# Optimization experiments

Hardware: AMD Instinct MI355X
Metric: run time of the kernel (lower is better)

Reference implementation:

```python
import jax, jax.numpy as jnp
import numpy as np

TAU = 2.0  # self.temperature
EPS = 1e-7

def setup_inputs() -> dict:
    key = jax.random.key(0)
    k1, k2, k3, k4, k5, k6 = jax.random.split(key, 6)
    B, S, H = 8, 4096, 512
    G, V, Dg = 2, 320, 128  # groups, codevectors per group, codevector_dim // G
    hidden_states = jax.random.normal(k1, (B, S, H), dtype=jnp.float32)
    mask_time_indices = jax.random.randint(k2, (B, S), 0, 2) > 0
    u = jax.random.uniform(k3, (B * S, G, V), dtype=jnp.float32, minval=1e-6, maxval=1.0 - 1e-6)
    gumbel_noise = -jnp.log(-jnp.log(u))  # standard Gumbel samples, as in F.gumbel_softmax
    W_proj = jax.random.normal(k4, (H, G * V), dtype=jnp.float32) * 0.02
    b_proj = jax.random.normal(k5, (G * V,), dtype=jnp.float32) * 0.02
    codevectors = jax.random.normal(k6, (G, V, Dg), dtype=jnp.float32)
    return {"hidden_states": hidden_states, "mask_time_indices": mask_time_indices,
            "gumbel_noise": gumbel_noise, "W_proj": W_proj, "b_proj": b_proj,
            "codevectors": codevectors}

def reference(hidden_states, mask_time_indices, gumbel_noise, W_proj, b_proj, codevectors):
    B, S, H = hidden_states.shape
    G, V, Dg = codevectors.shape
    N = B * S
    # weight projection: [B,S,H] -> [B,S,G*V] -> [N, G, V]
    logits = (jnp.einsum('bsh,hk->bsk', hidden_states, W_proj) + b_proj)
    logits = logits.reshape(N, G, V).astype(jnp.float32)
    # gumbel-softmax with hard=True (straight-through)
    y_soft = jax.nn.softmax((logits + gumbel_noise) / TAU, axis=-1)  # [N,G,V]
    idx = jnp.argmax(y_soft, axis=-1)                                 # [N,G]
    y_hard = jax.nn.one_hot(idx, V, dtype=y_soft.dtype)
    codevector_probs = y_hard + y_soft - jax.lax.stop_gradient(y_soft)
    # perplexity on the (noise-free) soft distribution, masked marginal
    soft_dist = jax.nn.softmax(logits, axis=-1)                       # [N,G,V]
    m = mask_time_indices.reshape(-1).astype(jnp.float32)             # [N]
    marginal = jnp.einsum('ngv,n->gv', soft_dist, m) / jnp.sum(m)
    perplexity = jnp.sum(jnp.exp(-jnp.sum(marginal * jnp.log(marginal + EPS), axis=-1)))
    # hard one-hot weighted sum over codebook == gather of selected codevector
    cv = jnp.einsum('ngv,gvd->ngd', codevector_probs, codevectors)    # [N,G,Dg]
    cv = cv.reshape(B, S, G * Dg)
    return cv, perplexity
```

## Files before the change

kernel.cpp:

```cpp
#include <hip/hip_runtime.h>
#include <hip/hip_bf16.h>
#include <math.h>

#define N_ROWS 32768
#define H      512
#define GV     640
#define V      320
#define DG     128
#define BM     32
#define NT     16

typedef __attribute__((ext_vector_type(4))) float f32x4;
typedef __attribute__((ext_vector_type(8))) short short8v;

static __device__ __forceinline__ short f2bf(float f) {
    unsigned int u = __float_as_uint(f);
    u += 0x7fffu + ((u >> 16) & 1u);
    return (short)(u >> 16);
}

__global__ __launch_bounds__(256)
void pack_w(const float* __restrict__ W, short* __restrict__ wp)
{
    int gid = blockIdx.x * 256 + threadIdx.x;
    int l   = gid & 63;
    int ct  = (gid >> 6) % 40;
    int t   = gid / (40 * 64);
    int row = t * 32 + 8 * (l >> 4);
    int col = ct * 16 + (l & 15);
    short8v pk;
    #pragma unroll
    for (int i = 0; i < 8; ++i)
        pk[i] = f2bf(W[(size_t)(row + i) * GV + col]);
    *(short8v*)(wp + (size_t)gid * 8) = pk;
}

__global__ __launch_bounds__(256)
void pack_a(const float* __restrict__ hidden, short* __restrict__ ap)
{
    int gid = blockIdx.x * 256 + threadIdx.x;
    int l   = gid & 63;
    int t   = (gid >> 6) & 15;
    int rt  = gid >> 10;
    const float* src = hidden + (size_t)(rt * 16 + (l & 15)) * H + t * 32 + 8 * (l >> 4);
    float4 x0 = *(const float4*)src;
    float4 x1 = *(const float4*)(src + 4);
    short8v pk;
    pk[0] = f2bf(x0.x); pk[1] = f2bf(x0.y); pk[2] = f2bf(x0.z); pk[3] = f2bf(x0.w);
    pk[4] = f2bf(x1.x); pk[5] = f2bf(x1.y); pk[6] = f2bf(x1.z); pk[7] = f2bf(x1.w);
    *(short8v*)(ap + (size_t)gid * 8) = pk;
}

__global__ __launch_bounds__(512, 4)
void gumbel_vq_main(const short* apack,
                    const int*   __restrict__ mask,
                    const float* __restrict__ gumbel,
                    const short* __restrict__ wpack,
                    const float* __restrict__ bias,
                    const float* __restrict__ codevec,
                    float* out,
                    float* __restrict__ ws)
{
    __shared__ __align__(16) short sbuf[2][20480];
    float4 (*ex)[16]  = (float4 (*)[16])(&sbuf[0][0]);
    float*  ex2       = (float*)((char*)sbuf + 2048);
    float*  mg        = (float*)((char*)sbuf + 2560);
    int   (*rowtab)[2] = (int (*)[2])((char*)sbuf + 7680);

    const int tid = threadIdx.x;
    const int tn  = tid & 63;
    const int wid = tid >> 6;
    const int wm  = wid >> 2;
    const int wn  = wid & 3;
    const int q   = tn >> 4;
    const int cn  = tn & 15;
    const int row0 = blockIdx.x * BM;
    const int cbase = wn * 160 + cn;

    f32x4 acc[10];
    #pragma unroll
    for (int j = 0; j < 10; ++j) {
        float b = bias[cbase + j * 16];
        f32x4 c; c[0] = b; c[1] = b; c[2] = b; c[3] = b;
        acc[j] = c;
    }

    const short* ab = apack + ((size_t)(blockIdx.x * 2 + wm) * NT * 64 + tn) * 8;

    {
        const short* wt = wpack;
        short8v s0 = *(const short8v*)(wt + (size_t)(tid +    0) * 8);
        short8v s1 = *(const short8v*)(wt + (size_t)(tid +  512) * 8);
        short8v s2 = *(const short8v*)(wt + (size_t)(tid + 1024) * 8);
        short8v s3 = *(const short8v*)(wt + (size_t)(tid + 1536) * 8);
        short8v s4 = *(const short8v*)(wt + (size_t)(tid + 2048) * 8);
        short* bd = &sbuf[0][(size_t)tid * 8];
        *(short8v*)(bd +     0) = s0;
        *(short8v*)(bd +  4096) = s1;
        *(short8v*)(bd +  8192) = s2;
        *(short8v*)(bd + 12288) = s3;
        *(short8v*)(bd + 16384) = s4;
    }
    short8v areg = *(const short8v*)ab;
    __syncthreads();

    #pragma unroll
    for (int t = 0; t < NT; ++t) {
        const int cur = t & 1;
        short8v s0, s1, s2, s3, s4, anx;
        if (t + 1 < NT) {
            const short* wt = wpack + (size_t)(t + 1) * 20480;
            s0 = *(const short8v*)(wt + (size_t)(tid +    0) * 8);
            s1 = *(const short8v*)(wt + (size_t)(tid +  512) * 8);
            s2 = *(const short8v*)(wt + (size_t)(tid + 1024) * 8);
            s3 = *(const short8v*)(wt + (size_t)(tid + 1536) * 8);
            s4 = *(const short8v*)(wt + (size_t)(tid + 2048) * 8);
            anx = *(const short8v*)(ab + (size_t)(t + 1) * 512);
        }
        const short* bufc = &sbuf[cur][(size_t)(wn * 640 + tn) * 8];
        #pragma unroll
        for (int j = 0; j < 10; ++j) {
            short8v bf = *(const short8v*)(bufc + j * 512);
            acc[j] = __builtin_amdgcn_mfma_f32_16x16x32_bf16(areg, bf, acc[j], 0, 0, 0);
        }
        if (t + 1 < NT) {
            short* bd = &sbuf[cur ^ 1][(size_t)tid * 8];
            *(short8v*)(bd +     0) = s0;
            *(short8v*)(bd +  4096) = s1;
            *(short8v*)(bd +  8192) = s2;
            *(short8v*)(bd + 12288) = s3;
            *(short8v*)(bd + 16384) = s4;
            areg = anx;
        }
        __syncthreads();
    }

    float g[4][10];
    #pragma unroll
    for (int r = 0; r < 4; ++r) {
        const float* gp = gumbel + (size_t)(row0 + wm * 16 + 4 * q + r) * GV + cbase;
        #pragma unroll
        for (int j = 0; j < 10; ++j) g[r][j] = gp[j * 16];
    }
    float mrow[4];
    #pragma unroll
    for (int r = 0; r < 4; ++r)
        mrow[r] = (mask[row0 + wm * 16 + 4 * q + r] != 0) ? 1.f : 0.f;

    float lm[4];
    #pragma unroll
    for (int r = 0; r < 4; ++r) {
        lm[r] = acc[0][r];
        #pragma unroll
        for (int j = 1; j < 10; ++j) lm[r] = fmaxf(lm[r], acc[j][r]);
    }
    #pragma unroll
    for (int d = 8; d >= 1; d >>= 1)
        #pragma unroll
        for (int r = 0; r < 4; ++r)
            lm[r] = fmaxf(lm[r], __shfl_xor(lm[r], d, 64));

    float zm[4]; int zi[4];
    #pragma unroll
    for (int r = 0; r < 4; ++r) {
        zm[r] = acc[0][r] + g[r][0]; zi[r] = cbase;
        #pragma unroll
        for (int j = 1; j < 10; ++j) {
            float zj = acc[j][r] + g[r][j];
            if (zj > zm[r]) { zm[r] = zj; zi[r] = cbase + 16 * j; }
        }
    }
    #pragma unroll
    for (int d = 8; d >= 1; d >>= 1) {
        #pragma unroll
        for (int r = 0; r < 4; ++r) {
            float oz = __shfl_xor(zm[r], d, 64); int oi = __shfl_xor(zi[r], d, 64);
            if (oz > zm[r] || (oz == zm[r] && oi < zi[r])) { zm[r] = oz; zi[r] = oi; }
        }
    }

    if (cn == 0) {
        #pragma unroll
        for (int r = 0; r < 4; ++r) {
            float4 e; e.x = zm[r]; e.y = __int_as_float(zi[r]); e.z = lm[r]; e.w = 0.f;
            ex[wid][4 * q + r] = e;
        }
    }
    __syncthreads();
    const int pw = wid ^ 1;
    #pragma unroll
    for (int r = 0; r < 4; ++r) {
        float4 e = ex[pw][4 * q + r];
        float pz = e.x; int pi = __float_as_int(e.y);
        if (pz > zm[r] || (pz == zm[r] && pi < zi[r])) { zm[r] = pz; zi[r] = pi; }
        lm[r] = fmaxf(lm[r], e.z);
    }

    float pm[4][10], ps[4];
    #pragma unroll
    for (int r = 0; r < 4; ++r) {
        ps[r] = 0.f;
        #pragma unroll
        for (int j = 0; j < 10; ++j) {
            float p = __expf(acc[j][r] - lm[r]);
            pm[r][j] = p; ps[r] += p;
        }
    }
    #pragma unroll
    for (int d = 8; d >= 1; d >>= 1)
        #pragma unroll
        for (int r = 0; r < 4; ++r)
            ps[r] += __shfl_xor(ps[r], d, 64);

    if (cn == 0) {
        #pragma unroll
        for (int r = 0; r < 4; ++r) ex2[wid * 16 + 4 * q + r] = ps[r];
    }
    __syncthreads();
    float inv[4];
    #pragma unroll
    for (int r = 0; r < 4; ++r)
        inv[r] = mrow[r] / (ps[r] + ex2[pw * 16 + 4 * q + r]);

    float part[10];
    #pragma unroll
    for (int j = 0; j < 10; ++j) {
        part[j] = pm[0][j] * inv[0] + pm[1][j] * inv[1] + pm[2][j] * inv[2] + pm[3][j] * inv[3];
        part[j] += __shfl_xor(part[j], 16, 64);
        part[j] += __shfl_xor(part[j], 32, 64);
    }
    if (q == 0) {
        #pragma unroll
        for (int j = 0; j < 10; ++j)
            mg[wm * GV + cbase + 16 * j] = part[j];
    }
    if ((wn == 0 || wn == 2) && cn == 0) {
        int grp = wn >> 1;
        #pragma unroll
        for (int r = 0; r < 4; ++r)
            rowtab[wm * 16 + 4 * q + r][grp] = zi[r] - grp * V;
    }
    __syncthreads();

    for (int c = tid; c < GV; c += 512)
        atomicAdd(&ws[c], mg[c] + mg[GV + c]);
    if (wid == 0) {
        int mr = (tn < BM) ? (mask[row0 + tn] != 0) : 0;
        unsigned long long b = __ballot(mr);
        if (tn == 0) atomicAdd(&ws[GV], (float)__popcll(b));
    }
    {
        const int row = tid >> 4;
        const int six = tid & 15;
        #pragma unroll
        for (int i = 0; i < 4; ++i) {
            int e4  = six + 16 * i;
            int grp = e4 >> 5;
            int off = e4 & 31;
            int idx = rowtab[row][grp];
            float4 vv = ((const float4*)(codevec + ((size_t)grp * V + idx) * DG))[off];
            ((float4*)(out + (size_t)(row0 + row) * (2 * DG)))[e4] = vv;
        }
    }
}

__global__ void gumbel_vq_finalize(const float* __restrict__ ws, float* __restrict__ out)
{
    __shared__ float red[GV];
    int t = threadIdx.x;
    float cnt = ws[GV];
    float p = ws[t] / cnt;
    red[t] = p * logf(p + 1e-7f);
    __syncthreads();
    if (t == 0) {
        float e0 = 0.f, e1 = 0.f;
        for (int i = 0; i < V; ++i)  e0 += red[i];
        for (int i = V; i < GV; ++i) e1 += red[i];
        out[(size_t)N_ROWS * 2 * DG] = expf(-e0) + expf(-e1);
    }
}

extern "C" void kernel_launch(void* const* d_in, const int* in_sizes, int n_in,
                              void* d_out, int out_size, void* d_ws, size_t ws_size,
                              hipStream_t stream)
{
    const float* hidden  = (const float*)d_in[0];
    const int*   mask    = (const int*)  d_in[1];
    const float* gumbel  = (const float*)d_in[2];
    const float* W       = (const float*)d_in[3];
    const float* bias    = (const float*)d_in[4];
    const float* codevec = (const float*)d_in[5];
    float* out = (float*)d_out;
    float* ws  = (float*)d_ws;
    short* wpack = (short*)((char*)d_ws + 4096);
    short* apack = (short*)d_out;

    hipMemsetAsync(d_ws, 0, (GV + 1) * sizeof(float), stream);
    pack_w<<<160, 256, 0, stream>>>(W, wpack);
    pack_a<<<8192, 256, 0, stream>>>(hidden, apack);
    gumbel_vq_main<<<N_ROWS / BM, 512, 0, stream>>>(apack, mask, gumbel, wpack, bias, codevec, out, ws);
    gumbel_vq_finalize<<<1, GV, 0, stream>>>(ws, out);
}
```

Baseline: 102.4 us.

## Process two 16-row tiles per wave to reuse LDS weight fragments

Doubles the rows per block from 32 to 64. Each wave now keeps two accumulator sets and runs two MFMAs on every weight fragment it reads from LDS, so the full packed weight matrix is streamed through LDS half as often per row. The softmax, argmax and marginal epilogue is looped over the two row tiles, and the codevector gather is remapped to cover 64 rows. The cost is more accumulator registers, which may lower occupancy, and half as many blocks to spread across CUs.

```diff
diff --git a/kernel.cpp b/kernel.cpp
--- a/kernel.cpp
+++ b/kernel.cpp
@@ -7,7 +7,7 @@
 #define GV     640
 #define V      320
 #define DG     128
-#define BM     32
+#define BM     64
 #define NT     16
 
 typedef __attribute__((ext_vector_type(4))) float f32x4;
@@ -62,9 +62,9 @@
                     float* __restrict__ ws)
 {
     __shared__ __align__(16) short sbuf[2][20480];
-    float4 (*ex)[16]  = (float4 (*)[16])(&sbuf[0][0]);
-    float*  ex2       = (float*)((char*)sbuf + 2048);
-    float*  mg        = (float*)((char*)sbuf + 2560);
+    float4 (*ex)[16]   = (float4 (*)[16])(&sbuf[0][0]);
+    float*  ex2        = (float*)((char*)sbuf + 2048);
+    float*  mg         = (float*)((char*)sbuf + 2560);
     int   (*rowtab)[2] = (int (*)[2])((char*)sbuf + 7680);
 
     const int tid = threadIdx.x;
@@ -77,15 +77,16 @@
     const int row0 = blockIdx.x * BM;
     const int cbase = wn * 160 + cn;
 
-    f32x4 acc[10];
+    f32x4 acc[2][10];
     #pragma unroll
     for (int j = 0; j < 10; ++j) {
         float b = bias[cbase + j * 16];
         f32x4 c; c[0] = b; c[1] = b; c[2] = b; c[3] = b;
-        acc[j] = c;
-    }
-
-    const short* ab = apack + ((size_t)(blockIdx.x * 2 + wm) * NT * 64 + tn) * 8;
+        acc[0][j] = c; acc[1][j] = c;
+    }
+
+    const short* ab0 = apack + ((size_t)(blockIdx.x * 4 + wm * 2) * 1024 + tn) * 8;
+    const short* ab1 = ab0 + (size_t)1024 * 8;
 
     {
         const short* wt = wpack;
@@ -101,13 +102,14 @@
         *(short8v*)(bd + 12288) = s3;
         *(short8v*)(bd + 16384) = s4;
     }
-    short8v areg = *(const short8v*)ab;
+    short8v areg0 = *(const short8v*)ab0;
+    short8v areg1 = *(const short8v*)ab1;
     __syncthreads();
 
     #pragma unroll
     for (int t = 0; t < NT; ++t) {
         const int cur = t & 1;
-        short8v s0, s1, s2, s3, s4, anx;
+        short8v s0, s1, s2, s3, s4, an0, an1;
         if (t + 1 < NT) {
             const short* wt = wpack + (size_t)(t + 1) * 20480;
             s0 = *(const short8v*)(wt + (size_t)(tid +    0) * 8);
@@ -115,13 +117,15 @@
             s2 = *(const short8v*)(wt + (size_t)(tid + 1024) * 8);
             s3 = *(const short8v*)(wt + (size_t)(tid + 1536) * 8);
             s4 = *(const short8v*)(wt + (size_t)(tid + 2048) * 8);
-            anx = *(const short8v*)(ab + (size_t)(t + 1) * 512);
+            an0 = *(const short8v*)(ab0 + (size_t)(t + 1) * 512);
+            an1 = *(const short8v*)(ab1 + (size_t)(t + 1) * 512);
         }
         const short* bufc = &sbuf[cur][(size_t)(wn * 640 + tn) * 8];
         #pragma unroll
         for (int j = 0; j < 10; ++j) {
             short8v bf = *(const short8v*)(bufc + j * 512);
-            acc[j] = __builtin_amdgcn_mfma_f32_16x16x32_bf16(areg, bf, acc[j], 0, 0, 0);
+            acc[0][j] = __builtin_amdgcn_mfma_f32_16x16x32_bf16(areg0, bf, acc[0][j], 0, 0, 0);
+            acc[1][j] = __builtin_amdgcn_mfma_f32_16x16x32_bf16(areg1, bf, acc[1][j], 0, 0, 0);
         }
         if (t + 1 < NT) {
             short* bd = &sbuf[cur ^ 1][(size_t)tid * 8];
@@ -130,102 +134,120 @@
             *(short8v*)(bd +  8192) = s2;
             *(short8v*)(bd + 12288) = s3;
             *(short8v*)(bd + 16384) = s4;
-            areg = anx;
+            areg0 = an0; areg1 = an1;
         }
         __syncthreads();
     }
 
-    float g[4][10];
-    #pragma unroll
-    for (int r = 0; r < 4; ++r) {
-        const float* gp = gumbel + (size_t)(row0 + wm * 16 + 4 * q + r) * GV + cbase;
-        #pragma unroll
-        for (int j = 0; j < 10; ++j) g[r][j] = gp[j * 16];
-    }
-    float mrow[4];
-    #pragma unroll
-    for (int r = 0; r < 4; ++r)
-        mrow[r] = (mask[row0 + wm * 16 + 4 * q + r] != 0) ? 1.f : 0.f;
-
-    float lm[4];
-    #pragma unroll
-    for (int r = 0; r < 4; ++r) {
-        lm[r] = acc[0][r];
-        #pragma unroll
-        for (int j = 1; j < 10; ++j) lm[r] = fmaxf(lm[r], acc[j][r]);
-    }
-    #pragma unroll
-    for (int d = 8; d >= 1; d >>= 1)
+    float part[10];
+    #pragma unroll
+    for (int j = 0; j < 10; ++j) part[j] = 0.f;
+    const int pw = wid ^ 1;
+
+    #pragma unroll
+    for (int rt = 0; rt < 2; ++rt) {
+        const int rowbase = row0 + wm * 32 + rt * 16;
+
+        float g[4][10];
+        #pragma unroll
+        for (int r = 0; r < 4; ++r) {
+            const float* gp = gumbel + (size_t)(rowbase + 4 * q + r) * GV + cbase;
+            #pragma unroll
+            for (int j = 0; j < 10; ++j) g[r][j] = gp[j * 16];
+        }
+        float mrow[4];
         #pragma unroll
         for (int r = 0; r < 4; ++r)
-            lm[r] = fmaxf(lm[r], __shfl_xor(lm[r], d, 64));
-
-    float zm[4]; int zi[4];
-    #pragma unroll
-    for (int r = 0; r < 4; ++r) {
-        zm[r] = acc[0][r] + g[r][0]; zi[r] = cbase;
-        #pragma unroll
-        for (int j = 1; j < 10; ++j) {
-            float zj = acc[j][r] + g[r][j];
-            if (zj > zm[r]) { zm[r] = zj; zi[r] = cbase + 16 * j; }
-        }
-    }
-    #pragma unroll
-    for (int d = 8; d >= 1; d >>= 1) {
-        #pragma unroll
-        for (int r = 0; r < 4; ++r) {
-            float oz = __shfl_xor(zm[r], d, 64); int oi = __shfl_xor(zi[r], d, 64);
-            if (oz > zm[r] || (oz == zm[r] && oi < zi[r])) { zm[r] = oz; zi[r] = oi; }
-        }
-    }
-
-    if (cn == 0) {
-        #pragma unroll
-        for (int r = 0; r < 4; ++r) {
-            float4 e; e.x = zm[r]; e.y = __int_as_float(zi[r]); e.z = lm[r]; e.w = 0.f;
-            ex[wid][4 * q + r] = e;
-        }
-    }
-    __syncthreads();
-    const int pw = wid ^ 1;
-    #pragma unroll
-    for (int r = 0; r < 4; ++r) {
-        float4 e = ex[pw][4 * q + r];
-        float pz = e.x; int pi = __float_as_int(e.y);
-        if (pz > zm[r] || (pz == zm[r] && pi < zi[r])) { zm[r] = pz; zi[r] = pi; }
-        lm[r] = fmaxf(lm[r], e.z);
-    }
-
-    float pm[4][10], ps[4];
-    #pragma unroll
-    for (int r = 0; r < 4; ++r) {
-        ps[r] = 0.f;
-        #pragma unroll
-        for (int j = 0; j < 10; ++j) {
-            float p = __expf(acc[j][r] - lm[r]);
-            pm[r][j] = p; ps[r] += p;
-        }
-    }
-    #pragma unroll
-    for (int d = 8; d >= 1; d >>= 1)
+            mrow[r] = (mask[rowbase + 4 * q + r] != 0) ? 1.f : 0.f;
+
+        float lm[4];
+        #pragma unroll
+        for (int r = 0; r < 4; ++r) {
+            lm[r] = acc[rt][0][r];
+            #pragma unroll
+            for (int j = 1; j < 10; ++j) lm[r] = fmaxf(lm[r], acc[rt][j][r]);
+        }
+        #pragma unroll
+        for (int d = 8; d >= 1; d >>= 1)
+            #pragma unroll
+            for (int r = 0; r < 4; ++r)
+                lm[r] = fmaxf(lm[r], __shfl_xor(lm[r], d, 64));
+
+        float zm[4]; int zi[4];
+        #pragma unroll
+        for (int r = 0; r < 4; ++r) {
+            zm[r] = acc[rt][0][r] + g[r][0]; zi[r] = cbase;
+            #pragma unroll
+            for (int j = 1; j < 10; ++j) {
+                float zj = acc[rt][j][r] + g[r][j];
+                if (zj > zm[r]) { zm[r] = zj; zi[r] = cbase + 16 * j; }
+            }
+        }
+        #pragma unroll
+        for (int d = 8; d >= 1; d >>= 1) {
+            #pragma unroll
+            for (int r = 0; r < 4; ++r) {
+                float oz = __shfl_xor(zm[r], d, 64); int oi = __shfl_xor(zi[r], d, 64);
+                if (oz > zm[r] || (oz == zm[r] && oi < zi[r])) { zm[r] = oz; zi[r] = oi; }
+            }
+        }
+
+        if (cn == 0) {
+            #pragma unroll
+            for (int r = 0; r < 4; ++r) {
+                float4 e; e.x = zm[r]; e.y = __int_as_float(zi[r]); e.z = lm[r]; e.w = 0.f;
+                ex[wid][4 * q + r] = e;
+            }
+        }
+        __syncthreads();
+        #pragma unroll
+        for (int r = 0; r < 4; ++r) {
+            float4 e = ex[pw][4 * q + r];
+            float pz = e.x; int pi = __float_as_int(e.y);
+            if (pz > zm[r] || (pz == zm[r] && pi < zi[r])) { zm[r] = pz; zi[r] = pi; }
+            lm[r] = fmaxf(lm[r], e.z);
+        }
+
+        float pm[4][10], ps[4];
+        #pragma unroll
+        for (int r = 0; r < 4; ++r) {
+            ps[r] = 0.f;
+            #pragma unroll
+            for (int j = 0; j < 10; ++j) {
+                float p = __expf(acc[rt][j][r] - lm[r]);
+                pm[r][j] = p; ps[r] += p;
+            }
+        }
+        #pragma unroll
+        for (int d = 8; d >= 1; d >>= 1)
+            #pragma unroll
+            for (int r = 0; r < 4; ++r)
+                ps[r] += __shfl_xor(ps[r], d, 64);
+
+        if (cn == 0) {
+            #pragma unroll
+            for (int r = 0; r < 4; ++r) ex2[wid * 16 + 4 * q + r] = ps[r];
+        }
+        __syncthreads();
+        float inv[4];
         #pragma unroll
         for (int r = 0; r < 4; ++r)
-            ps[r] += __shfl_xor(ps[r], d, 64);
-
-    if (cn == 0) {
-        #pragma unroll
-        for (int r = 0; r < 4; ++r) ex2[wid * 16 + 4 * q + r] = ps[r];
-    }
-    __syncthreads();
-    float inv[4];
-    #pragma unroll
-    for (int r = 0; r < 4; ++r)
-        inv[r] = mrow[r] / (ps[r] + ex2[pw * 16 + 4 * q + r]);
-
-    float part[10];
+            inv[r] = mrow[r] / (ps[r] + ex2[pw * 16 + 4 * q + r]);
+
+        #pragma unroll
+        for (int j = 0; j < 10; ++j)
+            part[j] += pm[0][j] * inv[0] + pm[1][j] * inv[1] + pm[2][j] * inv[2] + pm[3][j] * inv[3];
+
+        if ((wn == 0 || wn == 2) && cn == 0) {
+            int grp = wn >> 1;
+            #pragma unroll
+            for (int r = 0; r < 4; ++r)
+                rowtab[wm * 32 + rt * 16 + 4 * q + r][grp] = zi[r] - grp * V;
+        }
+    }
+
     #pragma unroll
     for (int j = 0; j < 10; ++j) {
-        part[j] = pm[0][j] * inv[0] + pm[1][j] * inv[1] + pm[2][j] * inv[2] + pm[3][j] * inv[3];
         part[j] += __shfl_xor(part[j], 16, 64);
         part[j] += __shfl_xor(part[j], 32, 64);
     }
@@ -233,28 +255,22 @@
         #pragma unroll
         for (int j = 0; j < 10; ++j)
             mg[wm * GV + cbase + 16 * j] = part[j];
-    }
-    if ((wn == 0 || wn == 2) && cn == 0) {
-        int grp = wn >> 1;
-        #pragma unroll
-        for (int r = 0; r < 4; ++r)
-            rowtab[wm * 16 + 4 * q + r][grp] = zi[r] - grp * V;
     }
     __syncthreads();
 
     for (int c = tid; c < GV; c += 512)
         atomicAdd(&ws[c], mg[c] + mg[GV + c]);
     if (wid == 0) {
-        int mr = (tn < BM) ? (mask[row0 + tn] != 0) : 0;
+        int mr = (mask[row0 + tn] != 0);
         unsigned long long b = __ballot(mr);
         if (tn == 0) atomicAdd(&ws[GV], (float)__popcll(b));
     }
     {
-        const int row = tid >> 4;
-        const int six = tid & 15;
-        #pragma unroll
-        for (int i = 0; i < 4; ++i) {
-            int e4  = six + 16 * i;
+        const int row = tid >> 3;
+        const int six = tid & 7;
+        #pragma unroll
+        for (int i = 0; i < 8; ++i) {
+            int e4  = six + 8 * i;
             int grp = e4 >> 5;
             int off = e4 & 31;
             int idx = rowtab[row][grp];
```

Measured after the change: 123.7 us. 1.21x slower.

## Double row tile to 64 rows per block with 1024 threads to share weight tiles

Applied to the files above, without the earlier changes.

Each block now covers 64 rows with 16 waves instead of 32 rows with 8 waves. Every weight K-tile staged in LDS is therefore reused by twice as many rows, which halves total global weight traffic and the number of blocks. Staging loads are spread over 1024 threads, and the marginal reduction now sums four per-wave partials. The cost is larger blocks with fewer resident per CU, since launch_bounds(1024,4) may force register limits, and the epilogue row-to-thread mapping must handle 64 rows.

```diff
diff --git a/kernel.cpp b/kernel.cpp
--- a/kernel.cpp
+++ b/kernel.cpp
@@ -7,7 +7,7 @@
 #define GV     640
 #define V      320
 #define DG     128
-#define BM     32
+#define BM     64
 #define NT     16
 
 typedef __attribute__((ext_vector_type(4))) float f32x4;
@@ -51,7 +51,7 @@
     *(short8v*)(ap + (size_t)gid * 8) = pk;
 }
 
-__global__ __launch_bounds__(512, 4)
+__global__ __launch_bounds__(1024, 4)
 void gumbel_vq_main(const short* apack,
                     const int*   __restrict__ mask,
                     const float* __restrict__ gumbel,
@@ -62,10 +62,10 @@
                     float* __restrict__ ws)
 {
     __shared__ __align__(16) short sbuf[2][20480];
-    float4 (*ex)[16]  = (float4 (*)[16])(&sbuf[0][0]);
-    float*  ex2       = (float*)((char*)sbuf + 2048);
-    float*  mg        = (float*)((char*)sbuf + 2560);
-    int   (*rowtab)[2] = (int (*)[2])((char*)sbuf + 7680);
+    float4 (*ex)[16]   = (float4 (*)[16])(&sbuf[0][0]);
+    float*  ex2        = (float*)((char*)sbuf + 4096);
+    float*  mg         = (float*)((char*)sbuf + 5120);
+    int   (*rowtab)[2] = (int (*)[2])((char*)sbuf + 15360);
 
     const int tid = threadIdx.x;
     const int tn  = tid & 63;
@@ -85,21 +85,20 @@
         acc[j] = c;
     }
 
-    const short* ab = apack + ((size_t)(blockIdx.x * 2 + wm) * NT * 64 + tn) * 8;
+    const short* ab = apack + ((size_t)(blockIdx.x * 4 + wm) * 1024 + tn) * 8;
+
+    const bool xtra = (tid < 512);
 
     {
         const short* wt = wpack;
         short8v s0 = *(const short8v*)(wt + (size_t)(tid +    0) * 8);
-        short8v s1 = *(const short8v*)(wt + (size_t)(tid +  512) * 8);
-        short8v s2 = *(const short8v*)(wt + (size_t)(tid + 1024) * 8);
-        short8v s3 = *(const short8v*)(wt + (size_t)(tid + 1536) * 8);
-        short8v s4 = *(const short8v*)(wt + (size_t)(tid + 2048) * 8);
+        short8v s1 = *(const short8v*)(wt + (size_t)(tid + 1024) * 8);
+        short8v s2;
+        if (xtra) s2 = *(const short8v*)(wt + (size_t)(tid + 2048) * 8);
         short* bd = &sbuf[0][(size_t)tid * 8];
         *(short8v*)(bd +     0) = s0;
-        *(short8v*)(bd +  4096) = s1;
-        *(short8v*)(bd +  8192) = s2;
-        *(short8v*)(bd + 12288) = s3;
-        *(short8v*)(bd + 16384) = s4;
+        *(short8v*)(bd +  8192) = s1;
+        if (xtra) *(short8v*)(bd + 16384) = s2;
     }
     short8v areg = *(const short8v*)ab;
     __syncthreads();
@@ -107,14 +106,12 @@
     #pragma unroll
     for (int t = 0; t < NT; ++t) {
         const int cur = t & 1;
-        short8v s0, s1, s2, s3, s4, anx;
+        short8v s0, s1, s2, anx;
         if (t + 1 < NT) {
             const short* wt = wpack + (size_t)(t + 1) * 20480;
             s0 = *(const short8v*)(wt + (size_t)(tid +    0) * 8);
-            s1 = *(const short8v*)(wt + (size_t)(tid +  512) * 8);
-            s2 = *(const short8v*)(wt + (size_t)(tid + 1024) * 8);
-            s3 = *(const short8v*)(wt + (size_t)(tid + 1536) * 8);
-            s4 = *(const short8v*)(wt + (size_t)(tid + 2048) * 8);
+            s1 = *(const short8v*)(wt + (size_t)(tid + 1024) * 8);
+            if (xtra) s2 = *(const short8v*)(wt + (size_t)(tid + 2048) * 8);
             anx = *(const short8v*)(ab + (size_t)(t + 1) * 512);
         }
         const short* bufc = &sbuf[cur][(size_t)(wn * 640 + tn) * 8];
@@ -126,26 +123,25 @@
         if (t + 1 < NT) {
             short* bd = &sbuf[cur ^ 1][(size_t)tid * 8];
             *(short8v*)(bd +     0) = s0;
-            *(short8v*)(bd +  4096) = s1;
-            *(short8v*)(bd +  8192) = s2;
-            *(short8v*)(bd + 12288) = s3;
-            *(short8v*)(bd + 16384) = s4;
+            *(short8v*)(bd +  8192) = s1;
+            if (xtra) *(short8v*)(bd + 16384) = s2;
             areg = anx;
         }
         __syncthreads();
     }
 
+    const int rowbase = row0 + wm * 16;
     float g[4][10];
     #pragma unroll
     for (int r = 0; r < 4; ++r) {
-        const float* gp = gumbel + (size_t)(row0 + wm * 16 + 4 * q + r) * GV + cbase;
+        const float* gp = gumbel + (size_t)(rowbase + 4 * q + r) * GV + cbase;
         #pragma unroll
         for (int j = 0; j < 10; ++j) g[r][j] = gp[j * 16];
     }
     float mrow[4];
     #pragma unroll
     for (int r = 0; r < 4; ++r)
-        mrow[r] = (mask[row0 + wm * 16 + 4 * q + r] != 0) ? 1.f : 0.f;
+        mrow[r] = (mask[rowbase + 4 * q + r] != 0) ? 1.f : 0.f;
 
     float lm[4];
     #pragma unroll
@@ -242,10 +238,10 @@
     }
     __syncthreads();
 
-    for (int c = tid; c < GV; c += 512)
-        atomicAdd(&ws[c], mg[c] + mg[GV + c]);
+    if (tid < GV)
+        atomicAdd(&ws[tid], mg[tid] + mg[GV + tid] + mg[2 * GV + tid] + mg[3 * GV + tid]);
     if (wid == 0) {
-        int mr = (tn < BM) ? (mask[row0 + tn] != 0) : 0;
+        int mr = (mask[row0 + tn] != 0);
         unsigned long long b = __ballot(mr);
         if (tn == 0) atomicAdd(&ws[GV], (float)__popcll(b));
     }
@@ -298,6 +294,6 @@
     hipMemsetAsync(d_ws, 0, (GV + 1) * sizeof(float), stream);
     pack_w<<<160, 256, 0, stream>>>(W, wpack);
     pack_a<<<8192, 256, 0, stream>>>(hidden, apack);
-    gumbel_vq_main<<<N_ROWS / BM, 512, 0, stream>>>(apack, mask, gumbel, wpack, bias, codevec, out, ws);
+    gumbel_vq_main<<<N_ROWS / BM, 1024, 0, stream>>>(apack, mask, gumbel, wpack, bias, codevec, out, ws);
     gumbel_vq_finalize<<<1, GV, 0, stream>>>(ws, out);
 }
```

New measurement: 93.91 us. 1.09x faster.
